# Performance work log

Measured on AMD Instinct MI355X. Metric: run time of the kernel, lower is better.

## Reference

```python
import jax, jax.numpy as jnp
import numpy as np

TOP_K = 2
EPS = 1e-9


def setup_inputs() -> dict:
    key = jax.random.key(0)
    k1, k2, k3, k4 = jax.random.split(key, 4)
    B, T, D, H, E = 4, 2048, 1024, 4096, 8
    x = jax.random.normal(k1, (B, T, D), dtype=jnp.float32)
    Wr = jax.random.normal(k2, (D, E), dtype=jnp.float32) * 0.02
    W1 = jax.random.normal(k3, (E, D, H), dtype=jnp.float32) * 0.02
    W2 = jax.random.normal(k4, (E, H, D), dtype=jnp.float32) * 0.02
    return {"x": x, "Wr": Wr, "W1": W1, "W2": W2}


def reference(x, Wr, W1, W2):
    # x: (B,T,D); Wr: (D,E); W1: (E,D,H); W2: (E,H,D)
    E = Wr.shape[1]
    logits = jnp.einsum('btd,de->bte', x, Wr)          # (B,T,E)
    probs = jax.nn.softmax(logits, axis=-1)
    top_p, top_i = jax.lax.top_k(probs, TOP_K)         # (B,T,K)
    gates = top_p / (jnp.sum(top_p, axis=-1, keepdims=True) + EPS)
    # combine weights per expert: (B,T,E), zero where expert not selected
    oh = jax.nn.one_hot(top_i, E, dtype=x.dtype)       # (B,T,K,E)
    comb = jnp.sum(oh * gates[..., None], axis=2)      # (B,T,E)
    out = jnp.zeros_like(x)
    for e in range(E):  # fixed small expert loop
        h = jax.nn.gelu(jnp.einsum('btd,dh->bth', x, W1[e]), approximate=False)
        y = jnp.einsum('bth,hd->btd', h, W2[e])
        out = out + comb[..., e:e + 1] * y
    # load-balancing loss (on detached stats, matching torch .detach())
    mask = (jnp.sum(oh, axis=2) > 0).astype(jnp.float32)  # (B,T,E)
    imp = jnp.sum(jax.lax.stop_gradient(probs), axis=(0, 1))
    load = jnp.sum(jax.lax.stop_gradient(mask), axis=(0, 1))
    imp = imp / (jnp.sum(imp) + EPS)
    load = load / (jnp.sum(load) + EPS)
    lb = jnp.sum(imp * load) * E
    return out, lb
```

## Files before the change

kernel.cpp:

```cpp
#include <hip/hip_runtime.h>
#include <hip/hip_bf16.h>
#include <math.h>

#define NTOK 8192
#define DDIM 1024
#define HDIM 4096
#define NEXP 8
#define HROWS (NTOK*2 + 256)
#define RBLK 512

typedef unsigned int u32;
typedef unsigned short u16;
typedef __bf16 bf16x8 __attribute__((ext_vector_type(8)));
typedef float f32x4 __attribute__((ext_vector_type(4)));
typedef u32 u32x4 __attribute__((ext_vector_type(4)));
typedef u16 u16x8 __attribute__((ext_vector_type(8)));
typedef u16 u16x4 __attribute__((ext_vector_type(4)));

__device__ __forceinline__ u16 f2bf(float f){
  u32 u = __builtin_bit_cast(u32, f);
  u32 r = (u + 0x7FFFu + ((u >> 16) & 1u)) >> 16;
  return (u16)r;
}
__device__ __forceinline__ float bf2f(u16 b){
  u32 u = ((u32)b) << 16;
  return __builtin_bit_cast(float, u);
}
__device__ __forceinline__ void gl_lds16(const void* g, void* l){
  __builtin_amdgcn_global_load_lds(
      (const __attribute__((address_space(1))) u32*)g,
      (__attribute__((address_space(3))) u32*)l, 16, 0, 0);
}
__device__ __forceinline__ float gelu_t(float v){
  float u = v * (0.7978845608f + 0.0356774081f * v * v);
  float e = __expf(2.0f * u);
  float t = 1.0f - 2.0f / (e + 1.0f);
  return 0.5f * v * (1.0f + t);
}

__global__ __launch_bounds__(256) void transpose_cvt(const float* __restrict__ in,
                                                     u16* __restrict__ out,
                                                     int R, int C){
  int e = blockIdx.z;
  const float* pin = in + (long)e * R * C;
  u16* pout = out + (long)e * R * C;
  __shared__ u16 tile[64][65];
  int c0 = blockIdx.x * 64, r0 = blockIdx.y * 64;
  int tid = threadIdx.x;
#pragma unroll
  for (int j = 0; j < 4; j++){
    int idx = tid + 256 * j;
    int r = idx >> 4, c4 = (idx & 15) << 2;
    float4 v = *(const float4*)(pin + (long)(r0 + r) * C + c0 + c4);
    tile[r][c4]     = f2bf(v.x);
    tile[r][c4 + 1] = f2bf(v.y);
    tile[r][c4 + 2] = f2bf(v.z);
    tile[r][c4 + 3] = f2bf(v.w);
  }
  __syncthreads();
#pragma unroll
  for (int j = 0; j < 4; j++){
    int idx = tid + 256 * j;
    int orow = idx >> 4, c4 = (idx & 15) << 2;
    u16x4 o;
    o[0] = tile[c4][orow];     o[1] = tile[c4 + 1][orow];
    o[2] = tile[c4 + 2][orow]; o[3] = tile[c4 + 3][orow];
    *(u16x4*)(pout + (long)(c0 + orow) * R + r0 + c4) = o;
  }
}

__global__ __launch_bounds__(1024) void route_kernel(const float* __restrict__ x,
                                                     const float* __restrict__ Wr,
                                                     u16* __restrict__ xb,
                                                     int4* __restrict__ meta,
                                                     float2* __restrict__ gates,
                                                     int* __restrict__ selrk,
                                                     int* __restrict__ blockhist,
                                                     float* __restrict__ impPart){
  const int wid = threadIdx.x >> 6;
  const int lane = threadIdx.x & 63;
  const int t = blockIdx.x * 16 + wid;
  const float* xr = x + (long)t * DDIM;
  u16* xbr = xb + (long)t * DDIM;
  float acc[NEXP] = {};
  for (int d0 = lane * 4; d0 < DDIM; d0 += 256){
    float4 xv = *(const float4*)(xr + d0);
    u16x4 xo;
    xo[0] = f2bf(xv.x); xo[1] = f2bf(xv.y); xo[2] = f2bf(xv.z); xo[3] = f2bf(xv.w);
    *(u16x4*)(xbr + d0) = xo;
    const float* w = Wr + d0 * NEXP;
#pragma unroll
    for (int q = 0; q < 4; q++){
      float xq = ((const float*)&xv)[q];
      float4 w0 = *(const float4*)(w + q * NEXP);
      float4 w1 = *(const float4*)(w + q * NEXP + 4);
      acc[0] += xq * w0.x; acc[1] += xq * w0.y; acc[2] += xq * w0.z; acc[3] += xq * w0.w;
      acc[4] += xq * w1.x; acc[5] += xq * w1.y; acc[6] += xq * w1.z; acc[7] += xq * w1.w;
    }
  }
#pragma unroll
  for (int e = 0; e < NEXP; e++){
#pragma unroll
    for (int off = 32; off; off >>= 1) acc[e] += __shfl_xor(acc[e], off, 64);
  }
  __shared__ int sel_s[32];
  __shared__ float p_s[16][NEXP];
  if (lane == 0){
    float mx = acc[0];
#pragma unroll
    for (int e = 1; e < NEXP; e++) mx = fmaxf(mx, acc[e]);
    float p[NEXP]; float s = 0.f;
#pragma unroll
    for (int e = 0; e < NEXP; e++){ p[e] = expf(acc[e] - mx); s += p[e]; }
    float inv = 1.f / s;
#pragma unroll
    for (int e = 0; e < NEXP; e++){ p[e] *= inv; p_s[wid][e] = p[e]; }
    int i0 = 0; float v0 = p[0];
#pragma unroll
    for (int e = 1; e < NEXP; e++) if (p[e] > v0){ v0 = p[e]; i0 = e; }
    int i1 = -1; float v1 = -1.f;
#pragma unroll
    for (int e = 0; e < NEXP; e++) if (e != i0 && p[e] > v1){ v1 = p[e]; i1 = e; }
    float gs = v0 + v1 + 1e-9f;
    meta[t] = make_int4(i0, i1, 0, 0);
    gates[t] = make_float2(v0 / gs, v1 / gs);
    sel_s[wid * 2] = i0;
    sel_s[wid * 2 + 1] = i1;
  }
  __syncthreads();
  const int tid = threadIdx.x;
  if (tid < 32){
    int e = sel_s[tid];
    int r = 0;
    for (int m = 0; m < tid; m++) r += (sel_s[m] == e) ? 1 : 0;
    selrk[blockIdx.x * 32 + tid] = (r << 3) | e;
  }
  if (tid < NEXP){
    int hcount = 0;
#pragma unroll
    for (int m = 0; m < 32; m++) hcount += (sel_s[m] == tid) ? 1 : 0;
    blockhist[blockIdx.x * NEXP + tid] = hcount;
    float s = 0.f;
#pragma unroll
    for (int w = 0; w < 16; w++) s += p_s[w][tid];
    impPart[blockIdx.x * NEXP + tid] = s;
  }
}

__global__ __launch_bounds__(512) void scan_kernel(int* __restrict__ blockhist,
                                                   const float* __restrict__ impPart,
                                                   int* __restrict__ cnt,
                                                   int* __restrict__ offs,
                                                   float* __restrict__ imp){
  const int e = threadIdx.x >> 6;
  const int lane = threadIdx.x & 63;
  const int base = lane * 8;
  int v[8]; int s = 0;
#pragma unroll
  for (int i = 0; i < 8; i++){
    int tmp = blockhist[(base + i) * NEXP + e];
    v[i] = s; s += tmp;
  }
  int inc = s;
#pragma unroll
  for (int off = 1; off < 64; off <<= 1){
    int o = __shfl_up(inc, off, 64);
    if (lane >= off) inc += o;
  }
  int excl = inc - s;
#pragma unroll
  for (int i = 0; i < 8; i++) blockhist[(base + i) * NEXP + e] = v[i] + excl;
  int tot = __shfl(inc, 63, 64);
  float fs = 0.f;
#pragma unroll
  for (int i = 0; i < 8; i++) fs += impPart[(base + i) * NEXP + e];
#pragma unroll
  for (int off = 32; off; off >>= 1) fs += __shfl_xor(fs, off, 64);
  __shared__ int cnt_s[NEXP];
  if (lane == 0){ cnt_s[e] = tot; cnt[e] = tot; imp[e] = fs; }
  __syncthreads();
  if (threadIdx.x == 0){
    int o = 0;
    for (int q = 0; q < NEXP; q++){ offs[q] = o; o += cnt_s[q]; }
  }
}

__global__ __launch_bounds__(256) void fill_kernel(const int* __restrict__ selrk,
                                                   const int* __restrict__ blockhist,
                                                   int* __restrict__ elist,
                                                   int4* __restrict__ meta){
  int m = blockIdx.x * 256 + threadIdx.x;
  int t = m >> 1, c = m & 1, b = m >> 5;
  int pk = selrk[m];
  int e = pk & 7, r = pk >> 3;
  int gslot = blockhist[b * NEXP + e] + r;
  elist[e * NTOK + gslot] = t;
  ((int*)meta)[t * 4 + 2 + c] = gslot;
}

template<int KD, int ND, bool GATHER, bool GELU>
__global__ __launch_bounds__(256, 2) void gemm_tb(const u16* __restrict__ Ag,
                                                  const u16* __restrict__ Bg,
                                                  u16* __restrict__ Cg,
                                                  const int* __restrict__ elist,
                                                  const int* __restrict__ cnt,
                                                  const int* __restrict__ offs){
  const int NDB = ND / 256;
  const int bid = blockIdx.x;
  const int e  = bid & 7;
  const int le = bid >> 3;
  const int db = le % NDB;
  const int tt = le / NDB;
  const int n_e = cnt[e];
  if (tt * 128 >= n_e) return;
  const int cb = db * 256;
  __shared__ __align__(16) u16 As[3][128 * 32];
  __shared__ __align__(16) u16 Bs[3][256 * 32];
  const int tid = threadIdx.x;
  const int sch = (((tid & 3) ^ ((tid >> 2) & 3) ^ ((tid >> 4) & 3)) << 3);
  const int row0 = offs[e] + tt * 128;
  long agb[2];
#pragma unroll
  for (int i = 0; i < 2; i++){
    int row = i * 64 + (tid >> 2);
    int arow;
    if (GATHER){
      int slot = tt * 128 + row;
      if (slot >= n_e) slot = n_e - 1;
      arow = elist[e * NTOK + slot];
    } else {
      arow = row0 + row;
    }
    agb[i] = (long)arow * KD + sch;
  }
  const long bbase = ((long)e * ND + cb) * KD;
  long bgb[4];
#pragma unroll
  for (int j = 0; j < 4; j++)
    bgb[j] = bbase + (long)(j * 64 + (tid >> 2)) * KD + sch;
  const int ldst = tid * 8;

  const int lane = tid & 63;
  const int w = tid >> 6;
  const int wc = w * 64;
  const int fr = lane & 15, fq = lane >> 4;
  const int swz = ((fq ^ (fr & 3) ^ ((fr >> 2) & 3)) << 4);
  const u32 aB0 = (u32)(uintptr_t)&As[0][0] + (u32)(fr * 64 + swz);
  const u32 bB0 = (u32)(uintptr_t)&Bs[0][0] + (u32)((wc + fr) * 64 + swz);

  f32x4 acc[8][4] = {};
  const int NK = KD / 32;

#define STG(cbuf, kel) \
    gl_lds16(Ag + agb[0] + (kel), &As[cbuf][0 * 2048 + ldst]); \
    gl_lds16(Ag + agb[1] + (kel), &As[cbuf][1 * 2048 + ldst]); \
    gl_lds16(Bg + bgb[0] + (kel), &Bs[cbuf][0 * 2048 + ldst]); \
    gl_lds16(Bg + bgb[1] + (kel), &Bs[cbuf][1 * 2048 + ldst]); \
    gl_lds16(Bg + bgb[2] + (kel), &Bs[cbuf][2 * 2048 + ldst]); \
    gl_lds16(Bg + bgb[3] + (kel), &Bs[cbuf][3 * 2048 + ldst]);

  STG(0, 0)
  STG(1, 32)
  asm volatile("s_waitcnt vmcnt(6)" ::: "memory");
  __builtin_amdgcn_s_barrier();

  int c = 0;
  for (int k = 0; k < NK; ++k){
    if (k + 2 < NK){
      int cn = c + 2; if (cn >= 3) cn -= 3;
      STG(cn, (k + 2) * 32)
    }
    const u32 aA = aB0 + (u32)(c * 8192);
    const u32 bA = bB0 + (u32)(c * 16384);
    u32x4 a[8], b[4];
    asm volatile("ds_read_b128 %0, %1"             : "=v"(a[0]) : "v"(aA));
    asm volatile("ds_read_b128 %0, %1 offset:1024" : "=v"(a[1]) : "v"(aA));
    asm volatile("ds_read_b128 %0, %1 offset:2048" : "=v"(a[2]) : "v"(aA));
    asm volatile("ds_read_b128 %0, %1 offset:3072" : "=v"(a[3]) : "v"(aA));
    asm volatile("ds_read_b128 %0, %1 offset:4096" : "=v"(a[4]) : "v"(aA));
    asm volatile("ds_read_b128 %0, %1 offset:5120" : "=v"(a[5]) : "v"(aA));
    asm volatile("ds_read_b128 %0, %1 offset:6144" : "=v"(a[6]) : "v"(aA));
    asm volatile("ds_read_b128 %0, %1 offset:7168" : "=v"(a[7]) : "v"(aA));
    asm volatile("ds_read_b128 %0, %1"             : "=v"(b[0]) : "v"(bA));
    asm volatile("ds_read_b128 %0, %1 offset:1024" : "=v"(b[1]) : "v"(bA));
    asm volatile("ds_read_b128 %0, %1 offset:2048" : "=v"(b[2]) : "v"(bA));
    asm volatile("ds_read_b128 %0, %1 offset:3072" : "=v"(b[3]) : "v"(bA));
    asm volatile("s_waitcnt lgkmcnt(0)" ::: "memory");
    __builtin_amdgcn_sched_barrier(0);
#pragma unroll
    for (int m = 0; m < 8; m++)
#pragma unroll
      for (int n = 0; n < 4; n++)
        acc[m][n] = __builtin_amdgcn_mfma_f32_16x16x32_bf16(
            __builtin_bit_cast(bf16x8, a[m]), __builtin_bit_cast(bf16x8, b[n]),
            acc[m][n], 0, 0, 0);
    if (k + 2 < NK){
      asm volatile("s_waitcnt vmcnt(6)" ::: "memory");
    } else if (k + 1 < NK){
      asm volatile("s_waitcnt vmcnt(0)" ::: "memory");
    }
    if (k + 1 < NK) __builtin_amdgcn_s_barrier();
    c += 1; if (c >= 3) c -= 3;
  }
#undef STG

#pragma unroll
  for (int m = 0; m < 8; m++){
#pragma unroll
    for (int j = 0; j < 4; j++){
      int row = m * 16 + fq * 4 + j;
      int slot = tt * 128 + row;
      if (slot >= n_e) continue;
      long base = (long)(row0 + row) * ND + cb + wc;
#pragma unroll
      for (int n = 0; n < 4; n++){
        float v = acc[m][n][j];
        if (GELU) v = gelu_t(v);
        Cg[base + n * 16 + fr] = f2bf(v);
      }
    }
  }
}

__global__ __launch_bounds__(256) void combine_kernel(const u16* __restrict__ ypair,
                                                      const int4* __restrict__ meta,
                                                      const float2* __restrict__ gates,
                                                      const int* __restrict__ offs,
                                                      float* __restrict__ out){
  int t = blockIdx.x;
  int c = threadIdx.x;
  int4 m = meta[t];
  float2 g = gates[t];
  long p0 = (long)(offs[m.x] + m.z) * DDIM + c * 4;
  long p1 = (long)(offs[m.y] + m.w) * DDIM + c * 4;
  u16x4 y0 = *(const u16x4*)&ypair[p0];
  u16x4 y1 = *(const u16x4*)&ypair[p1];
  float4 o;
  o.x = g.x * bf2f(y0[0]) + g.y * bf2f(y1[0]);
  o.y = g.x * bf2f(y0[1]) + g.y * bf2f(y1[1]);
  o.z = g.x * bf2f(y0[2]) + g.y * bf2f(y1[2]);
  o.w = g.x * bf2f(y0[3]) + g.y * bf2f(y1[3]);
  *(float4*)&out[(long)t * DDIM + c * 4] = o;
}

__global__ void lb_kernel(const float* __restrict__ imp, const int* __restrict__ cnt,
                          float* __restrict__ outp){
  if (threadIdx.x == 0 && blockIdx.x == 0){
    float si = 0.f, sl = 0.f;
    for (int e = 0; e < NEXP; e++){ si += imp[e]; sl += (float)cnt[e]; }
    float lb = 0.f;
    for (int e = 0; e < NEXP; e++)
      lb += (imp[e] / (si + 1e-9f)) * ((float)cnt[e] / (sl + 1e-9f));
    outp[0] = lb * (float)NEXP;
  }
}

extern "C" void kernel_launch(void* const* d_in, const int* in_sizes, int n_in,
                              void* d_out, int out_size, void* d_ws, size_t ws_size,
                              hipStream_t stream){
  const float* x  = (const float*)d_in[0];
  const float* Wr = (const float*)d_in[1];
  const float* W1 = (const float*)d_in[2];
  const float* W2 = (const float*)d_in[3];
  float* out = (float*)d_out;
  char* ws = (char*)d_ws;
  size_t off = 0;
  u16* xb = (u16*)(ws + off);   off += (size_t)NTOK * DDIM * 2;
  u16* wt = (u16*)(ws + off);   off += (size_t)NEXP * DDIM * HDIM * 2;
  u16* h  = (u16*)(ws + off);   off += (size_t)HROWS * HDIM * 2;
  u16* yp = (u16*)(ws + off);   off += (size_t)NTOK * 2 * DDIM * 2;
  int* elist    = (int*)(ws + off);    off += (size_t)NEXP * NTOK * 4;
  int4* meta    = (int4*)(ws + off);   off += (size_t)NTOK * 16;
  float2* gts   = (float2*)(ws + off); off += (size_t)NTOK * 8;
  int* selrk    = (int*)(ws + off);    off += (size_t)NTOK * 2 * 4;
  int* bhist    = (int*)(ws + off);    off += (size_t)RBLK * NEXP * 4;
  float* impP   = (float*)(ws + off);  off += (size_t)RBLK * NEXP * 4;
  int* cnt      = (int*)(ws + off);    off += 32;
  float* imp    = (float*)(ws + off);  off += 32;
  int* offs     = (int*)(ws + off);    off += 32;
  if (ws_size < off) return;

  route_kernel<<<RBLK, 1024, 0, stream>>>(x, Wr, xb, meta, gts, selrk, bhist, impP);
  scan_kernel<<<1, 512, 0, stream>>>(bhist, impP, cnt, offs, imp);
  fill_kernel<<<NTOK * 2 / 256, 256, 0, stream>>>(selrk, bhist, elist, meta);
  transpose_cvt<<<dim3(HDIM / 64, DDIM / 64, NEXP), 256, 0, stream>>>(W1, wt, DDIM, HDIM);
  gemm_tb<DDIM, HDIM, true, true><<<NEXP * (NTOK / 128) * (HDIM / 256), 256, 0, stream>>>(
      xb, wt, h, elist, cnt, offs);
  transpose_cvt<<<dim3(DDIM / 64, HDIM / 64, NEXP), 256, 0, stream>>>(W2, wt, HDIM, DDIM);
  gemm_tb<HDIM, DDIM, false, false><<<NEXP * (NTOK / 128) * (DDIM / 256), 256, 0, stream>>>(
      h, wt, yp, elist, cnt, offs);
  combine_kernel<<<NTOK, 256, 0, stream>>>(yp, meta, gts, offs, out);
  lb_kernel<<<1, 64, 0, stream>>>(imp, cnt, out + (size_t)NTOK * DDIM);
}
```

Baseline: 502.9 us.

## Switch MoE GEMMs to 32x32x16 MFMA and group token tiles for reuse

Replaces the 16x16x32 bf16 MFMA tiling with 32x32x16 MFMA, so each wave now does 4x2 larger tiles using fewer LDS reads per FLOP. LDS reads are split into two half-k batches so the second batch can overlap with the first set of MFMAs. Block index decoding now groups TG token tiles per weight column block, which is meant to improve L2 reuse of weight tiles. The epilogue is rewritten for the 32x32 accumulator layout, and the swizzle math changes, which risks LDS bank conflicts or indexing errors.

```diff
diff --git a/kernel.cpp b/kernel.cpp
--- a/kernel.cpp
+++ b/kernel.cpp
@@ -13,6 +13,7 @@
 typedef unsigned short u16;
 typedef __bf16 bf16x8 __attribute__((ext_vector_type(8)));
 typedef float f32x4 __attribute__((ext_vector_type(4)));
+typedef float f32x16 __attribute__((ext_vector_type(16)));
 typedef u32 u32x4 __attribute__((ext_vector_type(4)));
 typedef u16 u16x8 __attribute__((ext_vector_type(8)));
 typedef u16 u16x4 __attribute__((ext_vector_type(4)));
@@ -198,7 +199,7 @@
   ((int*)meta)[t * 4 + 2 + c] = gslot;
 }
 
-template<int KD, int ND, bool GATHER, bool GELU>
+template<int KD, int ND, int TG, bool GATHER, bool GELU>
 __global__ __launch_bounds__(256, 2) void gemm_tb(const u16* __restrict__ Ag,
                                                   const u16* __restrict__ Bg,
                                                   u16* __restrict__ Cg,
@@ -209,8 +210,10 @@
   const int bid = blockIdx.x;
   const int e  = bid & 7;
   const int le = bid >> 3;
-  const int db = le % NDB;
-  const int tt = le / NDB;
+  const int tti = le % TG;
+  const int db  = (le / TG) % NDB;
+  const int tg  = le / (TG * NDB);
+  const int tt  = tg * TG + tti;
   const int n_e = cnt[e];
   if (tt * 128 >= n_e) return;
   const int cb = db * 256;
@@ -240,15 +243,14 @@
     bgb[j] = bbase + (long)(j * 64 + (tid >> 2)) * KD + sch;
   const int ldst = tid * 8;
 
-  const int lane = tid & 63;
+  const int l = tid & 63;
   const int w = tid >> 6;
   const int wc = w * 64;
-  const int fr = lane & 15, fq = lane >> 4;
-  const int swz = ((fq ^ (fr & 3) ^ ((fr >> 2) & 3)) << 4);
-  const u32 aB0 = (u32)(uintptr_t)&As[0][0] + (u32)(fr * 64 + swz);
-  const u32 bB0 = (u32)(uintptr_t)&Bs[0][0] + (u32)((wc + fr) * 64 + swz);
-
-  f32x4 acc[8][4] = {};
+  const int s3 = (l & 3) ^ ((l >> 2) & 3);
+  const u32 aB0 = (u32)(uintptr_t)&As[0][0] + (u32)((l & 31) * 64 + ((((l >> 5)) ^ s3) << 4));
+  const u32 bB0 = (u32)(uintptr_t)&Bs[0][0] + (u32)((wc + (l & 31)) * 64 + ((((l >> 5)) ^ s3) << 4));
+
+  f32x16 acc[4][2] = {};
   const int NK = KD / 32;
 
 #define STG(cbuf, kel) \
@@ -272,28 +274,40 @@
     }
     const u32 aA = aB0 + (u32)(c * 8192);
     const u32 bA = bB0 + (u32)(c * 16384);
-    u32x4 a[8], b[4];
-    asm volatile("ds_read_b128 %0, %1"             : "=v"(a[0]) : "v"(aA));
-    asm volatile("ds_read_b128 %0, %1 offset:1024" : "=v"(a[1]) : "v"(aA));
-    asm volatile("ds_read_b128 %0, %1 offset:2048" : "=v"(a[2]) : "v"(aA));
-    asm volatile("ds_read_b128 %0, %1 offset:3072" : "=v"(a[3]) : "v"(aA));
-    asm volatile("ds_read_b128 %0, %1 offset:4096" : "=v"(a[4]) : "v"(aA));
-    asm volatile("ds_read_b128 %0, %1 offset:5120" : "=v"(a[5]) : "v"(aA));
-    asm volatile("ds_read_b128 %0, %1 offset:6144" : "=v"(a[6]) : "v"(aA));
-    asm volatile("ds_read_b128 %0, %1 offset:7168" : "=v"(a[7]) : "v"(aA));
-    asm volatile("ds_read_b128 %0, %1"             : "=v"(b[0]) : "v"(bA));
-    asm volatile("ds_read_b128 %0, %1 offset:1024" : "=v"(b[1]) : "v"(bA));
-    asm volatile("ds_read_b128 %0, %1 offset:2048" : "=v"(b[2]) : "v"(bA));
-    asm volatile("ds_read_b128 %0, %1 offset:3072" : "=v"(b[3]) : "v"(bA));
+    const u32 aA1 = aA ^ 32u;
+    const u32 bA1 = bA ^ 32u;
+    u32x4 a0[4], b0[2], a1[4], b1[2];
+    asm volatile("ds_read_b128 %0, %1"             : "=v"(a0[0]) : "v"(aA));
+    asm volatile("ds_read_b128 %0, %1 offset:2048" : "=v"(a0[1]) : "v"(aA));
+    asm volatile("ds_read_b128 %0, %1 offset:4096" : "=v"(a0[2]) : "v"(aA));
+    asm volatile("ds_read_b128 %0, %1 offset:6144" : "=v"(a0[3]) : "v"(aA));
+    asm volatile("ds_read_b128 %0, %1"             : "=v"(b0[0]) : "v"(bA));
+    asm volatile("ds_read_b128 %0, %1 offset:2048" : "=v"(b0[1]) : "v"(bA));
     asm volatile("s_waitcnt lgkmcnt(0)" ::: "memory");
     __builtin_amdgcn_sched_barrier(0);
-#pragma unroll
-    for (int m = 0; m < 8; m++)
-#pragma unroll
-      for (int n = 0; n < 4; n++)
-        acc[m][n] = __builtin_amdgcn_mfma_f32_16x16x32_bf16(
-            __builtin_bit_cast(bf16x8, a[m]), __builtin_bit_cast(bf16x8, b[n]),
-            acc[m][n], 0, 0, 0);
+    asm volatile("ds_read_b128 %0, %1"             : "=v"(a1[0]) : "v"(aA1));
+    asm volatile("ds_read_b128 %0, %1 offset:2048" : "=v"(a1[1]) : "v"(aA1));
+    asm volatile("ds_read_b128 %0, %1 offset:4096" : "=v"(a1[2]) : "v"(aA1));
+    asm volatile("ds_read_b128 %0, %1 offset:6144" : "=v"(a1[3]) : "v"(aA1));
+    asm volatile("ds_read_b128 %0, %1"             : "=v"(b1[0]) : "v"(bA1));
+    asm volatile("ds_read_b128 %0, %1 offset:2048" : "=v"(b1[1]) : "v"(bA1));
+    __builtin_amdgcn_sched_barrier(0);
+#pragma unroll
+    for (int ra = 0; ra < 4; ra++)
+#pragma unroll
+      for (int nb = 0; nb < 2; nb++)
+        acc[ra][nb] = __builtin_amdgcn_mfma_f32_32x32x16_bf16(
+            __builtin_bit_cast(bf16x8, a0[ra]), __builtin_bit_cast(bf16x8, b0[nb]),
+            acc[ra][nb], 0, 0, 0);
+    asm volatile("s_waitcnt lgkmcnt(0)" ::: "memory");
+    __builtin_amdgcn_sched_barrier(0);
+#pragma unroll
+    for (int ra = 0; ra < 4; ra++)
+#pragma unroll
+      for (int nb = 0; nb < 2; nb++)
+        acc[ra][nb] = __builtin_amdgcn_mfma_f32_32x32x16_bf16(
+            __builtin_bit_cast(bf16x8, a1[ra]), __builtin_bit_cast(bf16x8, b1[nb]),
+            acc[ra][nb], 0, 0, 0);
     if (k + 2 < NK){
       asm volatile("s_waitcnt vmcnt(6)" ::: "memory");
     } else if (k + 1 < NK){
@@ -305,18 +319,19 @@
 #undef STG
 
 #pragma unroll
-  for (int m = 0; m < 8; m++){
-#pragma unroll
-    for (int j = 0; j < 4; j++){
-      int row = m * 16 + fq * 4 + j;
+  for (int ra = 0; ra < 4; ra++){
+#pragma unroll
+    for (int reg = 0; reg < 16; reg++){
+      int r = (reg & 3) + 8 * (reg >> 2) + 4 * (l >> 5);
+      int row = ra * 32 + r;
       int slot = tt * 128 + row;
       if (slot >= n_e) continue;
-      long base = (long)(row0 + row) * ND + cb + wc;
-#pragma unroll
-      for (int n = 0; n < 4; n++){
-        float v = acc[m][n][j];
+      long base = (long)(row0 + row) * ND + cb + wc + (l & 31);
+#pragma unroll
+      for (int nb = 0; nb < 2; nb++){
+        float v = acc[ra][nb][reg];
         if (GELU) v = gelu_t(v);
-        Cg[base + n * 16 + fr] = f2bf(v);
+        Cg[base + nb * 32] = f2bf(v);
       }
     }
   }
@@ -384,10 +399,10 @@
   scan_kernel<<<1, 512, 0, stream>>>(bhist, impP, cnt, offs, imp);
   fill_kernel<<<NTOK * 2 / 256, 256, 0, stream>>>(selrk, bhist, elist, meta);
   transpose_cvt<<<dim3(HDIM / 64, DDIM / 64, NEXP), 256, 0, stream>>>(W1, wt, DDIM, HDIM);
-  gemm_tb<DDIM, HDIM, true, true><<<NEXP * (NTOK / 128) * (HDIM / 256), 256, 0, stream>>>(
+  gemm_tb<DDIM, HDIM, 8, true, true><<<NEXP * 64 * (HDIM / 256), 256, 0, stream>>>(
       xb, wt, h, elist, cnt, offs);
   transpose_cvt<<<dim3(DDIM / 64, HDIM / 64, NEXP), 256, 0, stream>>>(W2, wt, HDIM, DDIM);
-  gemm_tb<HDIM, DDIM, false, false><<<NEXP * (NTOK / 128) * (DDIM / 256), 256, 0, stream>>>(
+  gemm_tb<HDIM, DDIM, 2, false, false><<<NEXP * 64 * (DDIM / 256), 256, 0, stream>>>(
       h, wt, yp, elist, cnt, offs);
   combine_kernel<<<NTOK, 256, 0, stream>>>(yp, meta, gts, offs, out);
   lb_kernel<<<1, 64, 0, stream>>>(imp, cnt, out + (size_t)NTOK * DDIM);
```

Measured after the change: 539.2 us. +7.2%, slower.

## Use 512-thread GEMM blocks with 2x4 warp tiling and grouped block order

Applied to the files above, without the earlier changes.

The expert GEMM blocks go from 256 to 512 threads, with each wave now computing a 64x64 sub-tile in a 2x4 wave grid instead of 128x64. This halves per-wave accumulator registers and targets higher occupancy via launch_bounds(512,4). Block indices are also remapped so that TG consecutive token tiles share the same weight column block, aiming for better L2 reuse of weights. The global-to-LDS loads are redistributed over more threads and the wait counts are adjusted to match. The risk is lower MFMA work per LDS read for each wave.

```diff
diff --git a/kernel.cpp b/kernel.cpp
--- a/kernel.cpp
+++ b/kernel.cpp
@@ -198,8 +198,8 @@
   ((int*)meta)[t * 4 + 2 + c] = gslot;
 }
 
-template<int KD, int ND, bool GATHER, bool GELU>
-__global__ __launch_bounds__(256, 2) void gemm_tb(const u16* __restrict__ Ag,
+template<int KD, int ND, int TG, bool GATHER, bool GELU>
+__global__ __launch_bounds__(512, 4) void gemm_tb(const u16* __restrict__ Ag,
                                                   const u16* __restrict__ Bg,
                                                   u16* __restrict__ Cg,
                                                   const int* __restrict__ elist,
@@ -209,8 +209,10 @@
   const int bid = blockIdx.x;
   const int e  = bid & 7;
   const int le = bid >> 3;
-  const int db = le % NDB;
-  const int tt = le / NDB;
+  const int tti = le % TG;
+  const int db  = (le / TG) % NDB;
+  const int tg  = le / (TG * NDB);
+  const int tt  = tg * TG + tti;
   const int n_e = cnt[e];
   if (tt * 128 >= n_e) return;
   const int cb = db * 256;
@@ -219,10 +221,9 @@
   const int tid = threadIdx.x;
   const int sch = (((tid & 3) ^ ((tid >> 2) & 3) ^ ((tid >> 4) & 3)) << 3);
   const int row0 = offs[e] + tt * 128;
-  long agb[2];
-#pragma unroll
-  for (int i = 0; i < 2; i++){
-    int row = i * 64 + (tid >> 2);
+  long agb;
+  {
+    int row = tid >> 2;
     int arow;
     if (GATHER){
       int slot = tt * 128 + row;
@@ -231,37 +232,32 @@
     } else {
       arow = row0 + row;
     }
-    agb[i] = (long)arow * KD + sch;
+    agb = (long)arow * KD + sch;
   }
   const long bbase = ((long)e * ND + cb) * KD;
-  long bgb[4];
-#pragma unroll
-  for (int j = 0; j < 4; j++)
-    bgb[j] = bbase + (long)(j * 64 + (tid >> 2)) * KD + sch;
+  const long bgb0 = bbase + (long)(tid >> 2) * KD + sch;
+  const long bgb1 = bbase + (long)(128 + (tid >> 2)) * KD + sch;
   const int ldst = tid * 8;
 
-  const int lane = tid & 63;
+  const int l = tid & 63;
   const int w = tid >> 6;
-  const int wc = w * 64;
-  const int fr = lane & 15, fq = lane >> 4;
+  const int wm = w >> 2, wn = w & 3;
+  const int fr = l & 15, fq = l >> 4;
   const int swz = ((fq ^ (fr & 3) ^ ((fr >> 2) & 3)) << 4);
-  const u32 aB0 = (u32)(uintptr_t)&As[0][0] + (u32)(fr * 64 + swz);
-  const u32 bB0 = (u32)(uintptr_t)&Bs[0][0] + (u32)((wc + fr) * 64 + swz);
-
-  f32x4 acc[8][4] = {};
+  const u32 aB0 = (u32)(uintptr_t)&As[0][0] + (u32)((wm * 64 + fr) * 64 + swz);
+  const u32 bB0 = (u32)(uintptr_t)&Bs[0][0] + (u32)((wn * 64 + fr) * 64 + swz);
+
+  f32x4 acc[4][4] = {};
   const int NK = KD / 32;
 
 #define STG(cbuf, kel) \
-    gl_lds16(Ag + agb[0] + (kel), &As[cbuf][0 * 2048 + ldst]); \
-    gl_lds16(Ag + agb[1] + (kel), &As[cbuf][1 * 2048 + ldst]); \
-    gl_lds16(Bg + bgb[0] + (kel), &Bs[cbuf][0 * 2048 + ldst]); \
-    gl_lds16(Bg + bgb[1] + (kel), &Bs[cbuf][1 * 2048 + ldst]); \
-    gl_lds16(Bg + bgb[2] + (kel), &Bs[cbuf][2 * 2048 + ldst]); \
-    gl_lds16(Bg + bgb[3] + (kel), &Bs[cbuf][3 * 2048 + ldst]);
+    gl_lds16(Ag + agb + (kel), &As[cbuf][ldst]); \
+    gl_lds16(Bg + bgb0 + (kel), &Bs[cbuf][ldst]); \
+    gl_lds16(Bg + bgb1 + (kel), &Bs[cbuf][4096 + ldst]);
 
   STG(0, 0)
   STG(1, 32)
-  asm volatile("s_waitcnt vmcnt(6)" ::: "memory");
+  asm volatile("s_waitcnt vmcnt(3)" ::: "memory");
   __builtin_amdgcn_s_barrier();
 
   int c = 0;
@@ -272,15 +268,11 @@
     }
     const u32 aA = aB0 + (u32)(c * 8192);
     const u32 bA = bB0 + (u32)(c * 16384);
-    u32x4 a[8], b[4];
+    u32x4 a[4], b[4];
     asm volatile("ds_read_b128 %0, %1"             : "=v"(a[0]) : "v"(aA));
     asm volatile("ds_read_b128 %0, %1 offset:1024" : "=v"(a[1]) : "v"(aA));
     asm volatile("ds_read_b128 %0, %1 offset:2048" : "=v"(a[2]) : "v"(aA));
     asm volatile("ds_read_b128 %0, %1 offset:3072" : "=v"(a[3]) : "v"(aA));
-    asm volatile("ds_read_b128 %0, %1 offset:4096" : "=v"(a[4]) : "v"(aA));
-    asm volatile("ds_read_b128 %0, %1 offset:5120" : "=v"(a[5]) : "v"(aA));
-    asm volatile("ds_read_b128 %0, %1 offset:6144" : "=v"(a[6]) : "v"(aA));
-    asm volatile("ds_read_b128 %0, %1 offset:7168" : "=v"(a[7]) : "v"(aA));
     asm volatile("ds_read_b128 %0, %1"             : "=v"(b[0]) : "v"(bA));
     asm volatile("ds_read_b128 %0, %1 offset:1024" : "=v"(b[1]) : "v"(bA));
     asm volatile("ds_read_b128 %0, %1 offset:2048" : "=v"(b[2]) : "v"(bA));
@@ -288,14 +280,14 @@
     asm volatile("s_waitcnt lgkmcnt(0)" ::: "memory");
     __builtin_amdgcn_sched_barrier(0);
 #pragma unroll
-    for (int m = 0; m < 8; m++)
+    for (int m = 0; m < 4; m++)
 #pragma unroll
       for (int n = 0; n < 4; n++)
         acc[m][n] = __builtin_amdgcn_mfma_f32_16x16x32_bf16(
             __builtin_bit_cast(bf16x8, a[m]), __builtin_bit_cast(bf16x8, b[n]),
             acc[m][n], 0, 0, 0);
     if (k + 2 < NK){
-      asm volatile("s_waitcnt vmcnt(6)" ::: "memory");
+      asm volatile("s_waitcnt vmcnt(3)" ::: "memory");
     } else if (k + 1 < NK){
       asm volatile("s_waitcnt vmcnt(0)" ::: "memory");
     }
@@ -305,13 +297,13 @@
 #undef STG
 
 #pragma unroll
-  for (int m = 0; m < 8; m++){
+  for (int m = 0; m < 4; m++){
 #pragma unroll
     for (int j = 0; j < 4; j++){
-      int row = m * 16 + fq * 4 + j;
+      int row = wm * 64 + m * 16 + fq * 4 + j;
       int slot = tt * 128 + row;
       if (slot >= n_e) continue;
-      long base = (long)(row0 + row) * ND + cb + wc;
+      long base = (long)(row0 + row) * ND + cb + wn * 64;
 #pragma unroll
       for (int n = 0; n < 4; n++){
         float v = acc[m][n][j];
@@ -384,10 +376,10 @@
   scan_kernel<<<1, 512, 0, stream>>>(bhist, impP, cnt, offs, imp);
   fill_kernel<<<NTOK * 2 / 256, 256, 0, stream>>>(selrk, bhist, elist, meta);
   transpose_cvt<<<dim3(HDIM / 64, DDIM / 64, NEXP), 256, 0, stream>>>(W1, wt, DDIM, HDIM);
-  gemm_tb<DDIM, HDIM, true, true><<<NEXP * (NTOK / 128) * (HDIM / 256), 256, 0, stream>>>(
+  gemm_tb<DDIM, HDIM, 8, true, true><<<NEXP * 64 * (HDIM / 256), 512, 0, stream>>>(
       xb, wt, h, elist, cnt, offs);
   transpose_cvt<<<dim3(DDIM / 64, HDIM / 64, NEXP), 256, 0, stream>>>(W2, wt, HDIM, DDIM);
-  gemm_tb<HDIM, DDIM, false, false><<<NEXP * (NTOK / 128) * (DDIM / 256), 256, 0, stream>>>(
+  gemm_tb<HDIM, DDIM, 2, false, false><<<NEXP * 64 * (DDIM / 256), 512, 0, stream>>>(
       h, wt, yp, elist, cnt, offs);
   combine_kernel<<<NTOK, 256, 0, stream>>>(yp, meta, gts, offs, out);
   lb_kernel<<<1, 64, 0, stream>>>(imp, cnt, out + (size_t)NTOK * DDIM);
```

Result: slower. 517.2 us (+2.8%).
